# Performance work log

Measured on AMD Instinct MI355X. Metric: run time of the kernel, lower is better.

Reference implementation:

```python
import jax, jax.numpy as jnp
import numpy as np

B, L, S, H = 2, 256, 384, 768
Tc, Dc = 16, 50
WV, WD = 20000, 100
CV = 128
NEG = -1e30


def _lstm_scan(x, Wih, Whh, bih, bhh):
    # x: [N, T, D] -> hs: [N, T, Hc]; torch LSTM gate order i,f,g,o
    N = x.shape[0]
    Hc = Whh.shape[1]
    h0 = jnp.zeros((N, Hc), x.dtype)

    def step(carry, xt):
        h, c = carry
        g = xt @ Wih.T + h @ Whh.T + bih + bhh  # [N, 4Hc]
        i, f, gg, o = jnp.split(g, 4, axis=-1)
        i = jax.nn.sigmoid(i)
        f = jax.nn.sigmoid(f)
        gg = jnp.tanh(gg)
        o = jax.nn.sigmoid(o)
        c = f * c + i * gg
        h = o * jnp.tanh(c)
        return (h, c), h

    _, hs = jax.lax.scan(step, (h0, h0), jnp.swapaxes(x, 0, 1))
    return jnp.swapaxes(hs, 0, 1)


def setup_inputs() -> dict:
    key = jax.random.key(0)
    ks = jax.random.split(key, 10)
    bert_emb = jax.random.normal(ks[0], (B, S, H), jnp.float32)
    pieces2word = jax.random.randint(ks[1], (B, L, S), 0, 2, jnp.int32)
    word_ids = jax.random.randint(ks[2], (B, L), 0, WV, jnp.int32)
    char_count = jax.random.randint(ks[3], (B, L), 1, Tc + 1, jnp.int32)
    char_ids = jax.random.randint(ks[4], (B, L, Tc), 0, CV, jnp.int32)
    # mask consistent with ragged char lengths (first char_count positions valid)
    token_masks_char = (jnp.arange(Tc)[None, None, :] < char_count[..., None]).astype(jnp.int32)
    word_table = jax.random.normal(ks[5], (WV, WD), jnp.float32) * 0.02
    char_table = jax.random.normal(ks[6], (CV, Dc), jnp.float32) * 0.02
    sc = 1.0 / np.sqrt(Dc)

    def lstm_w(k):
        a, b, c, d = jax.random.split(k, 4)
        return (jax.random.uniform(a, (4 * Dc, Dc), jnp.float32, -sc, sc),
                jax.random.uniform(b, (4 * Dc, Dc), jnp.float32, -sc, sc),
                jax.random.uniform(c, (4 * Dc,), jnp.float32, -sc, sc),
                jax.random.uniform(d, (4 * Dc,), jnp.float32, -sc, sc))

    Wih_f, Whh_f, bih_f, bhh_f = lstm_w(ks[7])
    Wih_b, Whh_b, bih_b, bhh_b = lstm_w(ks[8])
    return dict(bert_emb=bert_emb, pieces2word=pieces2word, word_ids=word_ids,
                char_count=char_count, char_ids=char_ids, token_masks_char=token_masks_char,
                word_table=word_table, char_table=char_table,
                Wih_f=Wih_f, Whh_f=Whh_f, bih_f=bih_f, bhh_f=bhh_f,
                Wih_b=Wih_b, Whh_b=Whh_b, bih_b=bih_b, bhh_b=bhh_b)


def reference(bert_emb, pieces2word, word_ids, char_count, char_ids, token_masks_char,
              word_table, char_table, Wih_f, Whh_f, bih_f, bhh_f, Wih_b, Whh_b, bih_b, bhh_b):
    # --- piece2word max pool (expand + masked_fill(min) + max over pieces) ---
    minv = jnp.min(bert_emb)
    # [B, L, S, H] intermediate, as in the original expand
    masked = jnp.where(pieces2word[..., None] != 0, bert_emb[:, None, :, :], minv)
    word_reps = jnp.max(masked, axis=2)  # [B, L, H]
    # dropouts are identity in eval mode

    # --- word embedding lookup ---
    word_embed = word_table[word_ids]  # [B, L, WD]

    # --- char bi-LSTM with packed-sequence semantics ---
    lens = jnp.maximum(char_count.reshape(-1), 1)  # char_count[char_count==0]=1
    x = char_table[char_ids.reshape(B * L, Tc)]  # [N, Tc, Dc]
    h_fwd = _lstm_scan(x, Wih_f, Whh_f, bih_f, bhh_f)
    # reverse each sequence within its valid length for the backward direction
    t = jnp.arange(Tc)[None, :]
    idx = jnp.where(t < lens[:, None], lens[:, None] - 1 - t, t)  # [N, Tc]
    x_rev = jnp.take_along_axis(x, idx[..., None], axis=1)
    h_bwd = _lstm_scan(x_rev, Wih_b, Whh_b, bih_b, bhh_b)
    h_bwd = jnp.take_along_axis(h_bwd, idx[..., None], axis=1)  # back to original order
    h = jnp.concatenate([h_fwd, h_bwd], axis=-1)  # [N, Tc, 2*Dc]
    valid = (t < lens[:, None])[..., None]
    h = jnp.where(valid, h, 0.0)  # pad_packed_sequence zero-pads beyond length
    h = h.reshape(B, L, Tc, 2 * Dc)

    # --- combine(..., 'max'): masked max over ragged char groups ---
    m = jnp.where(token_masks_char[..., None] == 0, NEG, 0.0)
    sup = jnp.max(m + h, axis=2)  # [B, L, 2*Dc]
    sup = jnp.where(sup == NEG, 0.0, sup)

    return jnp.concatenate([word_reps, word_embed, sup], axis=-1)  # [B, L, H+WD+2*Dc]
```

## Files before the change

kernel.cpp:

```cpp
#include <hip/hip_runtime.h>
#include <float.h>

#define Bb 2
#define Ll 256
#define Ss 384
#define Hh 768
#define Tc 16
#define Dc 50
#define WD 100
#define CV 128
#define NG 200
#define OUTC 968
#define LT 8
#define NSC 4


__device__ inline float tanh_fast(float x) {
    float e = __expf(2.f * x);
    return 1.f - 2.f / (e + 1.f);
}
__device__ inline float sigmoid_fast(float x) {
    return 1.f / (1.f + __expf(-x));
}


__global__ __launch_bounds__(256) void kernelA(
        const float* __restrict__ bert, const int* __restrict__ p2w,
        const float* __restrict__ char_table,
        const float* __restrict__ Wih_f, const float* __restrict__ bih_f, const float* __restrict__ bhh_f,
        const float* __restrict__ Wih_b, const float* __restrict__ bih_b, const float* __restrict__ bhh_b,
        const int* __restrict__ word_ids, const float* __restrict__ word_table,
        float* __restrict__ minp, float* __restrict__ xpt, float* __restrict__ partial,
        float* __restrict__ out) {
    int blk = blockIdx.x, tid = threadIdx.x;
    if (blk < 256) {
        const int n = Bb * Ss * Hh;
        float m = FLT_MAX;
        for (int i = blk * 256 + tid; i < n; i += 256 * 256) m = fminf(m, bert[i]);
        #pragma unroll
        for (int off = 32; off; off >>= 1) m = fminf(m, __shfl_down(m, off, 64));
        __shared__ float red[4];
        if ((tid & 63) == 0) red[tid >> 6] = m;
        __syncthreads();
        if (tid == 0) minp[blk] = fminf(fminf(red[0], red[1]), fminf(red[2], red[3]));
    } else if (blk < 272) {
        int idx = blk - 256;
        int dir = idx >> 3, c0 = (idx & 7) * 16;
        const float* Wih = dir ? Wih_b : Wih_f;
        const float* bih = dir ? bih_b : bih_f;
        const float* bhh = dir ? bhh_b : bhh_f;
        __shared__ float ct[16][Dc];
        for (int e = tid; e < 16 * Dc; e += 256)
            ((float*)ct)[e] = char_table[c0 * Dc + e];
        __syncthreads();
        if (tid < NG) {
            float w[Dc];
            #pragma unroll
            for (int j = 0; j < Dc; j++) w[j] = Wih[tid * Dc + j];
            float bias = bih[tid] + bhh[tid];
            for (int cid = 0; cid < 16; cid++) {
                float a = bias;
                #pragma unroll
                for (int j = 0; j < Dc; j++) a += w[j] * ct[cid][j];
                xpt[(dir * CV + c0 + cid) * NG + tid] = a;
            }
        }
    } else if (blk < 336) {
        for (int i = (blk - 272) * 256 + tid; i < Bb * Ll * WD; i += 64 * 256) {
            int bl = i / WD, d = i - bl * WD;
            out[(size_t)bl * OUTC + Hh + d] = word_table[(size_t)word_ids[bl] * WD + d];
        }
    } else {
        int idx = blk - 336;
        int hc  = idx % 6;
        int lt  = (idx / 6) & 31;
        int bsc = idx / 192;
        int b   = bsc >> 2, sc = bsc & 3;
        int w    = tid >> 6;
        int lane = tid & 63;
        int s0 = sc * 96 + w * 24;

        const int* pm = p2w + ((size_t)(b * Ll + lt * LT)) * Ss + s0;
        unsigned m[LT];
        #pragma unroll
        for (int r = 0; r < LT; r++) {
            int v = (lane < 24) ? pm[r * Ss + lane] : 0;
            unsigned long long bal = __ballot(v != 0);
            m[r] = __builtin_amdgcn_readfirstlane((unsigned)bal);
        }

        const float2* bb2 = (const float2*)(bert + (size_t)b * Ss * Hh) + hc * 64 + lane;
        float2 acc[LT];
        #pragma unroll
        for (int r = 0; r < LT; r++) { acc[r].x = -FLT_MAX; acc[r].y = -FLT_MAX; }

        #pragma unroll
        for (int j = 0; j < 24; j++) {
            float2 v = bb2[(size_t)(s0 + j) * 384];
            #pragma unroll
            for (int r = 0; r < LT; r++) {
                if (m[r] & (1u << j)) {
                    acc[r].x = fmaxf(acc[r].x, v.x);
                    acc[r].y = fmaxf(acc[r].y, v.y);
                }
            }
        }

        __shared__ float sacc[4][LT][128];
        #pragma unroll
        for (int r = 0; r < LT; r++)
            *(float2*)&sacc[w][r][lane * 2] = acc[r];
        __syncthreads();

        for (int e = tid; e < LT * 128; e += 256) {
            int r = e >> 7, c = e & 127;
            float m0 = fmaxf(fmaxf(sacc[0][r][c], sacc[1][r][c]),
                             fmaxf(sacc[2][r][c], sacc[3][r][c]));
            size_t row = (size_t)b * Ll + lt * LT + r;
            partial[((size_t)sc * (Bb * Ll) + row) * Hh + hc * 128 + c] = m0;
        }
    }
}


__global__ __launch_bounds__(256) void kernelB(
        const int* __restrict__ char_ids, const int* __restrict__ char_count,
        const float* __restrict__ Whh_f, const float* __restrict__ Whh_b,
        const float* __restrict__ xpt, const float* __restrict__ partial,
        const float* __restrict__ minp, float* __restrict__ out) {
    int blk = blockIdx.x, tid = threadIdx.x;
    if (blk < 1024) {
        int n = blk >> 1, dir = blk & 1;
        const float* Whh = dir ? Whh_b : Whh_f;

        __shared__ float xg[Tc][NG];
        __shared__ float gs[NG];
        __shared__ __align__(16) float hs[52];
        __shared__ int scid[Tc];

        int len = char_count[n];
        if (len < 1) len = 1;
        if (tid < Tc) {
            int t = tid;
            int st = dir ? (t < len ? len - 1 - t : t) : t;
            scid[t] = char_ids[n * Tc + st];
        }
        if (tid < 52) hs[tid] = 0.f;
        __syncthreads();

        for (int e = tid; e < Tc * NG; e += 256) {
            int t = e / NG, g = e - t * NG;
            xg[t][g] = xpt[(dir * CV + scid[t]) * NG + g];
        }
        float w[52];
        if (tid < NG) {
            #pragma unroll
            for (int j = 0; j < Dc; j++) w[j] = Whh[tid * Dc + j];
            w[50] = 0.f; w[51] = 0.f;
        }
        __syncthreads();

        float c = 0.f, maxv = -FLT_MAX;
        for (int t = 0; t < Tc; t++) {
            if (tid < NG) {
                float g = xg[t][tid];
                #pragma unroll
                for (int j = 0; j < 52; j += 4) {
                    float4 hv = *(const float4*)&hs[j];
                    g += hv.x * w[j] + hv.y * w[j+1] + hv.z * w[j+2] + hv.w * w[j+3];
                }
                gs[tid] = g;
            }
            __syncthreads();
            if (tid < Dc) {
                float si = sigmoid_fast(gs[tid]);
                float sf = sigmoid_fast(gs[tid + 50]);
                float tg = tanh_fast(gs[tid + 100]);
                float so = sigmoid_fast(gs[tid + 150]);
                c = sf * c + si * tg;
                float h = so * tanh_fast(c);
                hs[tid] = h;
                if (t < len) maxv = fmaxf(maxv, h);
            }
            __syncthreads();
        }
        if (tid < Dc)
            out[(size_t)n * OUTC + (Hh + WD) + dir * Dc + tid] = maxv;
    } else {
        __shared__ float sminv;
        if (tid < 64) {
            float m = fminf(fminf(minp[tid], minp[tid + 64]),
                            fminf(minp[tid + 128], minp[tid + 192]));
            #pragma unroll
            for (int off = 32; off; off >>= 1) m = fminf(m, __shfl_down(m, off, 64));
            if (tid == 0) sminv = m;
        }
        __syncthreads();
        float mv = sminv;
        const int TOT = Bb * Ll * Hh;
        for (int e = (blk - 1024) * 256 + tid; e < TOT; e += 384 * 256) {
            float m = fmaxf(fmaxf(partial[e], partial[TOT + e]),
                            fmaxf(partial[2 * TOT + e], partial[3 * TOT + e]));
            if (m == -FLT_MAX) m = mv;
            int row = e / Hh, c = e - row * Hh;
            out[(size_t)row * OUTC + c] = m;
        }
    }
}

extern "C" void kernel_launch(void* const* d_in, const int* in_sizes, int n_in,
                              void* d_out, int out_size, void* d_ws, size_t ws_size,
                              hipStream_t stream) {
    const float* bert       = (const float*)d_in[0];
    const int*   p2w        = (const int*)d_in[1];
    const int*   word_ids   = (const int*)d_in[2];
    const int*   char_count = (const int*)d_in[3];
    const int*   char_ids   = (const int*)d_in[4];
    const float* word_table = (const float*)d_in[6];
    const float* char_table = (const float*)d_in[7];
    const float* Wih_f = (const float*)d_in[8];
    const float* Whh_f = (const float*)d_in[9];
    const float* bih_f = (const float*)d_in[10];
    const float* bhh_f = (const float*)d_in[11];
    const float* Wih_b = (const float*)d_in[12];
    const float* Whh_b = (const float*)d_in[13];
    const float* bih_b = (const float*)d_in[14];
    const float* bhh_b = (const float*)d_in[15];
    float* out = (float*)d_out;

    float* minp    = (float*)d_ws;
    float* xpt     = minp + 256;
    float* partial = xpt + 2 * CV * NG;

    kernelA<<<1872, 256, 0, stream>>>(
        bert, p2w, char_table, Wih_f, bih_f, bhh_f, Wih_b, bih_b, bhh_b,
        word_ids, word_table, minp, xpt, partial, out);
    kernelB<<<1408, 256, 0, stream>>>(
        char_ids, char_count, Whh_f, Whh_b, xpt, partial, minp, out);
}
```

Measured before the change: 130.1 us.

## Run each LSTM sequence in one wavefront with register-held weights and prefetch

The char BiLSTM is remapped so each wavefront handles one (sequence, direction) pair. Each lane owns one hidden unit and computes all four of its gates from register-resident Whh rows, which removes the block-wide __syncthreads and the shared gate buffer at every timestep. The next step's precomputed input projections are prefetched through shuffled char ids, so the shared-memory staging pass goes away. Kernel A also gains a float4 min-reduction over half as many blocks and finer Wih-projection blocks, and the max-combine tail runs fixed 4-element chunks per block. The trade-off is heavy register pressure (about 208 weight floats per lane) under launch_bounds(256,1), and the inter-lane hidden-state exchange through LDS now relies on wavefront lockstep without explicit barriers.

New measurement: 128.5 us. About the same (-1.3%).

```diff
diff --git a/kernel.cpp b/kernel.cpp
--- a/kernel.cpp
+++ b/kernel.cpp
@@ -12,7 +12,7 @@
 #define NG 200
 #define OUTC 968
 #define LT 8
-#define NSC 4
+#define TOT (Bb * Ll * Hh)
 
 
 __device__ inline float tanh_fast(float x) {
@@ -33,45 +33,49 @@
         float* __restrict__ minp, float* __restrict__ xpt, float* __restrict__ partial,
         float* __restrict__ out) {
     int blk = blockIdx.x, tid = threadIdx.x;
-    if (blk < 256) {
-        const int n = Bb * Ss * Hh;
+    if (blk < 128) {
+        const int n4 = (Bb * Ss * Hh) / 4;
+        const float4* b4 = (const float4*)bert;
         float m = FLT_MAX;
-        for (int i = blk * 256 + tid; i < n; i += 256 * 256) m = fminf(m, bert[i]);
+        for (int i = blk * 256 + tid; i < n4; i += 128 * 256) {
+            float4 v = b4[i];
+            m = fminf(m, fminf(fminf(v.x, v.y), fminf(v.z, v.w)));
+        }
         #pragma unroll
         for (int off = 32; off; off >>= 1) m = fminf(m, __shfl_down(m, off, 64));
         __shared__ float red[4];
         if ((tid & 63) == 0) red[tid >> 6] = m;
         __syncthreads();
         if (tid == 0) minp[blk] = fminf(fminf(red[0], red[1]), fminf(red[2], red[3]));
-    } else if (blk < 272) {
-        int idx = blk - 256;
-        int dir = idx >> 3, c0 = (idx & 7) * 16;
+    } else if (blk < 192) {
+        int idx = blk - 128;
+        int dir = idx >> 5, c0 = (idx & 31) * 4;
         const float* Wih = dir ? Wih_b : Wih_f;
         const float* bih = dir ? bih_b : bih_f;
         const float* bhh = dir ? bhh_b : bhh_f;
-        __shared__ float ct[16][Dc];
-        for (int e = tid; e < 16 * Dc; e += 256)
-            ((float*)ct)[e] = char_table[c0 * Dc + e];
+        __shared__ float ct[4][Dc];
+        if (tid < 4 * Dc) ((float*)ct)[tid] = char_table[c0 * Dc + tid];
         __syncthreads();
         if (tid < NG) {
             float w[Dc];
             #pragma unroll
             for (int j = 0; j < Dc; j++) w[j] = Wih[tid * Dc + j];
             float bias = bih[tid] + bhh[tid];
-            for (int cid = 0; cid < 16; cid++) {
+            #pragma unroll
+            for (int cid = 0; cid < 4; cid++) {
                 float a = bias;
                 #pragma unroll
                 for (int j = 0; j < Dc; j++) a += w[j] * ct[cid][j];
                 xpt[(dir * CV + c0 + cid) * NG + tid] = a;
             }
         }
-    } else if (blk < 336) {
-        for (int i = (blk - 272) * 256 + tid; i < Bb * Ll * WD; i += 64 * 256) {
+    } else if (blk < 256) {
+        for (int i = (blk - 192) * 256 + tid; i < Bb * Ll * WD; i += 64 * 256) {
             int bl = i / WD, d = i - bl * WD;
             out[(size_t)bl * OUTC + Hh + d] = word_table[(size_t)word_ids[bl] * WD + d];
         }
     } else {
-        int idx = blk - 336;
+        int idx = blk - 256;
         int hc  = idx % 6;
         int lt  = (idx / 6) & 31;
         int bsc = idx / 192;
@@ -123,82 +127,100 @@
 }
 
 
-__global__ __launch_bounds__(256) void kernelB(
+__global__ __launch_bounds__(256, 1) void kernelB(
         const int* __restrict__ char_ids, const int* __restrict__ char_count,
         const float* __restrict__ Whh_f, const float* __restrict__ Whh_b,
         const float* __restrict__ xpt, const float* __restrict__ partial,
         const float* __restrict__ minp, float* __restrict__ out) {
     int blk = blockIdx.x, tid = threadIdx.x;
-    if (blk < 1024) {
-        int n = blk >> 1, dir = blk & 1;
+    int wv = tid >> 6, lane = tid & 63;
+
+    if (blk < 256) {
+        __shared__ __align__(16) float hs[4][52];
+        float* hsw = hs[wv];
+
+        int wid = blk * 4 + wv;
+        int n = wid >> 1, dir = wid & 1;
         const float* Whh = dir ? Whh_b : Whh_f;
-
-        __shared__ float xg[Tc][NG];
-        __shared__ float gs[NG];
-        __shared__ __align__(16) float hs[52];
-        __shared__ int scid[Tc];
 
         int len = char_count[n];
         if (len < 1) len = 1;
-        if (tid < Tc) {
-            int t = tid;
-            int st = dir ? (t < len ? len - 1 - t : t) : t;
-            scid[t] = char_ids[n * Tc + st];
-        }
-        if (tid < 52) hs[tid] = 0.f;
-        __syncthreads();
-
-        for (int e = tid; e < Tc * NG; e += 256) {
-            int t = e / NG, g = e - t * NG;
-            xg[t][g] = xpt[(dir * CV + scid[t]) * NG + g];
-        }
-        float w[52];
-        if (tid < NG) {
-            #pragma unroll
-            for (int j = 0; j < Dc; j++) w[j] = Whh[tid * Dc + j];
-            w[50] = 0.f; w[51] = 0.f;
-        }
-        __syncthreads();
-
-        float c = 0.f, maxv = -FLT_MAX;
+
+        int cidv = 0;
+        if (lane < Tc) {
+            int st = dir ? (lane < len ? len - 1 - lane : lane) : lane;
+            cidv = char_ids[n * Tc + st];
+        }
+
+        float w[4][52];
+        if (lane < Dc) {
+            #pragma unroll
+            for (int q = 0; q < 4; q++) {
+                const float2* wr = (const float2*)(Whh + (q * Dc + lane) * Dc);
+                #pragma unroll
+                for (int mm = 0; mm < 25; mm++) {
+                    float2 t = wr[mm];
+                    w[q][2 * mm] = t.x; w[q][2 * mm + 1] = t.y;
+                }
+            }
+        }
+        #pragma unroll
+        for (int q = 0; q < 4; q++) { w[q][50] = 0.f; w[q][51] = 0.f; }
+
+        if (lane < 52) hsw[lane] = 0.f;
+
+        int cid0 = __shfl(cidv, 0);
+        const float* xr = xpt + (size_t)(dir * CV + cid0) * NG;
+        float xp[4];
+        #pragma unroll
+        for (int q = 0; q < 4; q++) xp[q] = (lane < Dc) ? xr[q * Dc + lane] : 0.f;
+
+        float c = 0.f, h = 0.f, maxv = -FLT_MAX;
         for (int t = 0; t < Tc; t++) {
-            if (tid < NG) {
-                float g = xg[t][tid];
-                #pragma unroll
-                for (int j = 0; j < 52; j += 4) {
-                    float4 hv = *(const float4*)&hs[j];
-                    g += hv.x * w[j] + hv.y * w[j+1] + hv.z * w[j+2] + hv.w * w[j+3];
-                }
-                gs[tid] = g;
-            }
-            __syncthreads();
-            if (tid < Dc) {
-                float si = sigmoid_fast(gs[tid]);
-                float sf = sigmoid_fast(gs[tid + 50]);
-                float tg = tanh_fast(gs[tid + 100]);
-                float so = sigmoid_fast(gs[tid + 150]);
+            int tn = (t + 1 < Tc) ? t + 1 : t;
+            int cidn = __shfl(cidv, tn);
+            const float* xrn = xpt + (size_t)(dir * CV + cidn) * NG;
+            float xpn[4];
+            #pragma unroll
+            for (int q = 0; q < 4; q++) xpn[q] = (lane < Dc) ? xrn[q * Dc + lane] : 0.f;
+
+            float g0 = xp[0], g1 = xp[1], g2 = xp[2], g3 = xp[3];
+            #pragma unroll
+            for (int mm = 0; mm < 13; mm++) {
+                float4 hv = *(const float4*)&hsw[4 * mm];
+                g0 += hv.x * w[0][4*mm] + hv.y * w[0][4*mm+1] + hv.z * w[0][4*mm+2] + hv.w * w[0][4*mm+3];
+                g1 += hv.x * w[1][4*mm] + hv.y * w[1][4*mm+1] + hv.z * w[1][4*mm+2] + hv.w * w[1][4*mm+3];
+                g2 += hv.x * w[2][4*mm] + hv.y * w[2][4*mm+1] + hv.z * w[2][4*mm+2] + hv.w * w[2][4*mm+3];
+                g3 += hv.x * w[3][4*mm] + hv.y * w[3][4*mm+1] + hv.z * w[3][4*mm+2] + hv.w * w[3][4*mm+3];
+            }
+            if (lane < Dc) {
+                float si = sigmoid_fast(g0);
+                float sf = sigmoid_fast(g1);
+                float tg = tanh_fast(g2);
+                float so = sigmoid_fast(g3);
                 c = sf * c + si * tg;
-                float h = so * tanh_fast(c);
-                hs[tid] = h;
+                h = so * tanh_fast(c);
                 if (t < len) maxv = fmaxf(maxv, h);
-            }
-            __syncthreads();
-        }
-        if (tid < Dc)
-            out[(size_t)n * OUTC + (Hh + WD) + dir * Dc + tid] = maxv;
+                hsw[lane] = h;
+            }
+            #pragma unroll
+            for (int q = 0; q < 4; q++) xp[q] = xpn[q];
+        }
+        if (lane < Dc)
+            out[(size_t)n * OUTC + (Hh + WD) + dir * Dc + lane] = maxv;
     } else {
         __shared__ float sminv;
         if (tid < 64) {
-            float m = fminf(fminf(minp[tid], minp[tid + 64]),
-                            fminf(minp[tid + 128], minp[tid + 192]));
+            float m = fminf(minp[tid], minp[tid + 64]);
             #pragma unroll
             for (int off = 32; off; off >>= 1) m = fminf(m, __shfl_down(m, off, 64));
             if (tid == 0) sminv = m;
         }
         __syncthreads();
         float mv = sminv;
-        const int TOT = Bb * Ll * Hh;
-        for (int e = (blk - 1024) * 256 + tid; e < TOT; e += 384 * 256) {
+        int e = (blk - 256) * 1024 + tid;
+        #pragma unroll
+        for (int k = 0; k < 4; k++, e += 256) {
             float m = fmaxf(fmaxf(partial[e], partial[TOT + e]),
                             fmaxf(partial[2 * TOT + e], partial[3 * TOT + e]));
             if (m == -FLT_MAX) m = mv;
@@ -229,12 +251,12 @@
     float* out = (float*)d_out;
 
     float* minp    = (float*)d_ws;
-    float* xpt     = minp + 256;
+    float* xpt     = minp + 128;
     float* partial = xpt + 2 * CV * NG;
 
-    kernelA<<<1872, 256, 0, stream>>>(
+    kernelA<<<1792, 256, 0, stream>>>(
         bert, p2w, char_table, Wih_f, bih_f, bhh_f, Wih_b, bih_b, bhh_b,
         word_ids, word_table, minp, xpt, partial, out);
-    kernelB<<<1408, 256, 0, stream>>>(
+    kernelB<<<640, 256, 0, stream>>>(
         char_ids, char_count, Whh_f, Whh_b, xpt, partial, minp, out);
 }
```
